# Performance work log

Measured on AMD Instinct MI355X. Metric: run time of the kernel, lower is better.

Reference implementation:

```python
import jax, jax.numpy as jnp
import numpy as np

B, T, D = 2, 2048, 2048
H, KVH, HD = 32, 8, 64
N_REP = H // KVH


def setup_inputs() -> dict:
    key = jax.random.key(0)
    ks = jax.random.split(key, 7)
    x = jax.random.normal(ks[0], (B, T, D), dtype=jnp.float32)
    # rope tables: [max_seq, head_dim//2]
    cos = jax.random.uniform(ks[1], (T, HD // 2), dtype=jnp.float32, minval=-1.0, maxval=1.0)
    sin = jax.random.uniform(ks[2], (T, HD // 2), dtype=jnp.float32, minval=-1.0, maxval=1.0)
    s = 0.02
    wq = jax.random.normal(ks[3], (D, H * HD), dtype=jnp.float32) * s
    wk = jax.random.normal(ks[4], (D, KVH * HD), dtype=jnp.float32) * s
    wv = jax.random.normal(ks[5], (D, KVH * HD), dtype=jnp.float32) * s
    wo = jax.random.normal(ks[6], (H * HD, D), dtype=jnp.float32) * s
    return {"x": x, "cos": cos, "sin": sin, "wq": wq, "wk": wk, "wv": wv, "wo": wo}


def _rotate(t):
    h = t.shape[-1] // 2
    return jnp.concatenate([-t[..., h:], t[..., :h]], axis=-1)


def reference(x, cos, sin, wq, wk, wv, wo):
    b, t, _ = x.shape
    # projections -> [B, heads, T, HD]
    q = (x @ wq).reshape(b, t, H, HD).transpose(0, 2, 1, 3)
    k = (x @ wk).reshape(b, t, KVH, HD).transpose(0, 2, 1, 3)
    v = (x @ wv).reshape(b, t, KVH, HD).transpose(0, 2, 1, 3)
    # rope: cos/sin tiled (concat) to full head_dim, broadcast over batch/head
    cos_f = jnp.tile(cos[:t], (1, 2))[None, None]  # [1,1,T,HD]
    sin_f = jnp.tile(sin[:t], (1, 2))[None, None]
    q = q * cos_f + _rotate(q) * sin_f
    k = k * cos_f + _rotate(k) * sin_f
    # GQA: repeat kv heads
    k = jnp.repeat(k, N_REP, axis=1)
    v = jnp.repeat(v, N_REP, axis=1)
    scale = 1.0 / np.sqrt(HD).astype(np.float32)
    scores = jnp.einsum('bhqd,bhkd->bhqk', q, k) * scale
    causal = jnp.tril(jnp.ones((t, t), dtype=bool))
    scores = jnp.where(causal, scores, jnp.float32(-1e30))
    attn = jax.nn.softmax(scores, axis=-1)
    out = jnp.einsum('bhqk,bhkd->bhqd', attn, v)
    out = out.transpose(0, 2, 1, 3).reshape(b, t, H * HD)
    return out @ wo
```

## Files before the change

kernel.cpp:

```cpp
#include <hip/hip_runtime.h>
#include <hip/hip_bf16.h>
#include <cstdint>

typedef unsigned short u16;
typedef unsigned int u32;
typedef __bf16 bf16x8 __attribute__((ext_vector_type(8)));
typedef float f32x4 __attribute__((ext_vector_type(4)));

#define BATCH 2
#define SEQ 2048
#define DMODEL 2048
#define NH 32
#define NKVH 8
#define HD 64
#define NQROWS (BATCH*SEQ)
#define QCOLS (NH*HD)
#define KVCOLS (NKVH*HD)
#define NCAT (QCOLS+2*KVCOLS)

static __device__ __forceinline__ u16 f2bf(float f) {
  u32 u = __float_as_uint(f);
  return (u16)((u + 0x7fffu + ((u >> 16) & 1u)) >> 16);
}

#define GLOAD16(gp, lp) __builtin_amdgcn_global_load_lds( \
    (const __attribute__((address_space(1))) void*)(gp),  \
    (__attribute__((address_space(3))) void*)(lp), 16, 0, 0)

__global__ __launch_bounds__(256) void k_cvt_bf16(const float* __restrict__ in,
                                                  u16* __restrict__ out, int n4) {
  int i = blockIdx.x * 256 + threadIdx.x;
  if (i >= n4) return;
  float4 v = reinterpret_cast<const float4*>(in)[i];
  ushort4 o;
  o.x = f2bf(v.x); o.y = f2bf(v.y); o.z = f2bf(v.z); o.w = f2bf(v.w);
  reinterpret_cast<ushort4*>(out)[i] = o;
}

__global__ __launch_bounds__(256) void k_transpose_w(const float* __restrict__ in,
                                                     u16* __restrict__ out, int R, int C) {
  __shared__ float tile[32][33];
  int c0 = blockIdx.x * 32, r0 = blockIdx.y * 32;
  int tx = threadIdx.x, ty = threadIdx.y;
#pragma unroll
  for (int i = 0; i < 4; i++)
    tile[ty * 4 + i][tx] = in[(size_t)(r0 + ty * 4 + i) * C + c0 + tx];
  __syncthreads();
#pragma unroll
  for (int i = 0; i < 4; i++)
    out[(size_t)(c0 + ty * 4 + i) * R + r0 + tx] = f2bf(tile[tx][ty * 4 + i]);
}

template<int EPI>
__global__ __launch_bounds__(256) void k_gemm(const u16* __restrict__ A,
                                              const u16* __restrict__ BT,
                                              void* __restrict__ Cout,
                                              int M, int N, int K,
                                              const float* __restrict__ cosb,
                                              const float* __restrict__ sinb,
                                              u16* __restrict__ dstK,
                                              u16* __restrict__ dstV) {
  __shared__ __align__(16) u16 As[128 * 32];
  __shared__ __align__(16) u16 Bs[128 * 32];
  const int tid = threadIdx.x;
  const int w = tid >> 6, l = tid & 63;
  const int l15 = l & 15, l4 = l >> 4;
  const int m0 = blockIdx.y * 128, n0 = blockIdx.x * 128;
  const int wr = w >> 1, wc = w & 1;

  const u16* ga = A + (size_t)(m0 + w * 32 + (l >> 2)) * K + (l & 3) * 8;
  const u16* gb = BT + (size_t)(n0 + w * 32 + (l >> 2)) * K + (l & 3) * 8;
  u16* asb = &As[w * 1024];
  u16* bsb = &Bs[w * 1024];
  const int af_off = (wr * 64 + l15) * 32 + l4 * 8;
  const int bf_off = (wc * 64 + l15) * 32 + l4 * 8;

  f32x4 acc[4][4] = {};
  for (int kt = 0; kt < K; kt += 32) {
    GLOAD16(ga, asb);
    GLOAD16(ga + 16 * (size_t)K, asb + 512);
    GLOAD16(gb, bsb);
    GLOAD16(gb + 16 * (size_t)K, bsb + 512);
    ga += 32; gb += 32;
    __syncthreads();
    bf16x8 af[4], bfv[4];
#pragma unroll
    for (int mi = 0; mi < 4; mi++)
      af[mi] = *reinterpret_cast<const bf16x8*>(&As[af_off + mi * 512]);
#pragma unroll
    for (int ni = 0; ni < 4; ni++)
      bfv[ni] = *reinterpret_cast<const bf16x8*>(&Bs[bf_off + ni * 512]);
#pragma unroll
    for (int mi = 0; mi < 4; mi++)
#pragma unroll
      for (int ni = 0; ni < 4; ni++)
        acc[mi][ni] = __builtin_amdgcn_mfma_f32_16x16x32_bf16(af[mi], bfv[ni], acc[mi][ni], 0, 0, 0);
    __syncthreads();
  }

  const int row0 = m0 + wr * 64 + l4 * 4;
  const int col0 = n0 + wc * 64 + l15;
  if constexpr (EPI == 1) {
    float* C = (float*)Cout;
#pragma unroll
    for (int mi = 0; mi < 4; mi++)
#pragma unroll
      for (int ni = 0; ni < 4; ni++)
#pragma unroll
        for (int j = 0; j < 4; j++)
          C[(size_t)(row0 + mi * 16 + j) * N + col0 + ni * 16] = acc[mi][ni][j];
  } else {
    if (n0 < QCOLS + KVCOLS) {
#pragma unroll
      for (int mi = 0; mi < 4; mi++)
#pragma unroll
        for (int j = 0; j < 4; j++) {
          int t = (row0 + mi * 16 + j) & (SEQ - 1);
#pragma unroll
          for (int ni = 0; ni < 2; ni++) {
            int d = ni * 16 + l15;
            float c = cosb[t * 32 + d], s = sinb[t * 32 + d];
            float a = acc[mi][ni][j], bb = acc[mi][ni + 2][j];
            acc[mi][ni][j]     = a * c - bb * s;
            acc[mi][ni + 2][j] = bb * c + a * s;
          }
        }
      if (n0 < QCOLS) {
        u16* C = (u16*)Cout;
#pragma unroll
        for (int mi = 0; mi < 4; mi++)
#pragma unroll
          for (int ni = 0; ni < 4; ni++)
#pragma unroll
            for (int j = 0; j < 4; j++)
              C[(size_t)(row0 + mi * 16 + j) * QCOLS + col0 + ni * 16] = f2bf(acc[mi][ni][j]);
      } else {
        int kc0 = col0 - QCOLS;
#pragma unroll
        for (int mi = 0; mi < 4; mi++)
#pragma unroll
          for (int ni = 0; ni < 4; ni++)
#pragma unroll
            for (int j = 0; j < 4; j++)
              dstK[(size_t)(row0 + mi * 16 + j) * KVCOLS + kc0 + ni * 16] = f2bf(acc[mi][ni][j]);
      }
    } else {
      int vc0 = col0 - (QCOLS + KVCOLS);
#pragma unroll
      for (int mi = 0; mi < 4; mi++) {
        int row = row0 + mi * 16;
        int b = row >> 11, t = row & (SEQ - 1);
#pragma unroll
        for (int ni = 0; ni < 4; ni++) {
          ushort4 v;
          v.x = f2bf(acc[mi][ni][0]);
          v.y = f2bf(acc[mi][ni][1]);
          v.z = f2bf(acc[mi][ni][2]);
          v.w = f2bf(acc[mi][ni][3]);
          *reinterpret_cast<ushort4*>(&dstV[((size_t)b * KVCOLS + vc0 + ni * 16) * SEQ + t]) = v;
        }
      }
    }
  }
}

__global__ __launch_bounds__(256) void k_attn(const u16* __restrict__ Q,
                                              const u16* __restrict__ K,
                                              const u16* __restrict__ VT,
                                              u16* __restrict__ AO) {
  __shared__ __align__(16) u16 Ks[2][4096];
  __shared__ __align__(16) u16 Vs[2][4096];
  __shared__ __align__(16) u16 Plds[4][16][72];
  const int tid = threadIdx.x;
  const int w = tid >> 6, l = tid & 63;
  const int l15 = l & 15, l4 = l >> 4;
  const int bh = blockIdx.y;
  const int b = bh >> 5, h = bh & 31, g = h >> 2;
  const float cS = 0.125f * 1.44269504088896f;
  const int srow_w = w * 8 + (l >> 3);
  const int sslot = l & 7;

  const u16* Kbase = K + ((size_t)b * SEQ) * KVCOLS + g * 64;
  const u16* Vbase = VT + ((size_t)(b * KVCOLS + g * 64)) * SEQ;

  for (int half = 0; half < 2; half++) {
    const int qt = half ? (31 - blockIdx.x) : blockIdx.x;
    const int qrow0 = qt * 64 + w * 16;
    const int nkc = qt + 1;

    bf16x8 aQ[2];
    {
      const u16* qp = Q + (size_t)(b * SEQ + qrow0 + l15) * QCOLS + h * 64 + l4 * 8;
      aQ[0] = *reinterpret_cast<const bf16x8*>(qp);
      aQ[1] = *reinterpret_cast<const bf16x8*>(qp + 32);
    }
    f32x4 oacc[4] = {};
    float lsumP[4] = {};

#pragma unroll
    for (int i = 0; i < 2; i++) {
      int r = i * 32 + srow_w;
      int cs = sslot ^ (r & 7);
      GLOAD16(Kbase + (size_t)r * KVCOLS + cs * 8, &Ks[0][i * 2048 + w * 512 + l * 8]);
      GLOAD16(Vbase + (size_t)r * SEQ + cs * 8, &Vs[0][i * 2048 + w * 512 + l * 8]);
    }
    __syncthreads();

    for (int kc = 0; kc < nkc; kc++) {
      const int bi = kc & 1;
      if (kc + 1 < nkc) {
#pragma unroll
        for (int i = 0; i < 2; i++) {
          int r = i * 32 + srow_w;
          int cs = sslot ^ (r & 7);
          GLOAD16(Kbase + (size_t)((kc + 1) * 64 + r) * KVCOLS + cs * 8,
                  &Ks[bi ^ 1][i * 2048 + w * 512 + l * 8]);
          GLOAD16(Vbase + (size_t)r * SEQ + (kc + 1) * 64 + cs * 8,
                  &Vs[bi ^ 1][i * 2048 + w * 512 + l * 8]);
        }
      }
      f32x4 sacc[4] = {};
#pragma unroll
      for (int ni = 0; ni < 4; ni++) {
        int kr = ni * 16 + l15;
#pragma unroll
        for (int hh = 0; hh < 2; hh++) {
          int slot = (hh * 4 + l4) ^ (kr & 7);
          bf16x8 kf = *reinterpret_cast<const bf16x8*>(&Ks[bi][kr * 64 + slot * 8]);
          sacc[ni] = __builtin_amdgcn_mfma_f32_16x16x32_bf16(aQ[hh], kf, sacc[ni], 0, 0, 0);
        }
      }
      const bool diag = (kc == qt);
      {
        int qr = qrow0 + l4 * 4;
#pragma unroll
        for (int ni = 0; ni < 4; ni++) {
          int kcol = kc * 64 + ni * 16 + l15;
#pragma unroll
          for (int j = 0; j < 4; j++) {
            float pv = exp2f(sacc[ni][j] * cS);
            if (diag && (kcol > qr + j)) pv = 0.f;
            lsumP[j] += pv;
            __bf16 pb = (__bf16)pv;
            Plds[w][l4 * 4 + j][ni * 16 + l15] = *(u16*)&pb;
          }
        }
      }
      {
        bf16x8 pa0 = *reinterpret_cast<const bf16x8*>(&Plds[w][l15][l4 * 8]);
        bf16x8 pa1 = *reinterpret_cast<const bf16x8*>(&Plds[w][l15][32 + l4 * 8]);
#pragma unroll
        for (int no = 0; no < 4; no++) {
          int vr = no * 16 + l15;
          int s0 = l4 ^ (vr & 7);
          int s1 = (4 + l4) ^ (vr & 7);
          bf16x8 v0 = *reinterpret_cast<const bf16x8*>(&Vs[bi][vr * 64 + s0 * 8]);
          bf16x8 v1 = *reinterpret_cast<const bf16x8*>(&Vs[bi][vr * 64 + s1 * 8]);
          oacc[no] = __builtin_amdgcn_mfma_f32_16x16x32_bf16(pa0, v0, oacc[no], 0, 0, 0);
          oacc[no] = __builtin_amdgcn_mfma_f32_16x16x32_bf16(pa1, v1, oacc[no], 0, 0, 0);
        }
      }
      __syncthreads();
    }
#pragma unroll
    for (int j = 0; j < 4; j++) {
      float v = lsumP[j];
      v += __shfl_xor(v, 1, 16);
      v += __shfl_xor(v, 2, 16);
      v += __shfl_xor(v, 4, 16);
      v += __shfl_xor(v, 8, 16);
      float rv = 1.f / v;
      int row = b * SEQ + qrow0 + l4 * 4 + j;
#pragma unroll
      for (int no = 0; no < 4; no++)
        AO[(size_t)row * QCOLS + h * 64 + no * 16 + l15] = f2bf(oacc[no][j] * rv);
    }
  }
}

extern "C" void kernel_launch(void* const* d_in, const int* in_sizes, int n_in,
                              void* d_out, int out_size, void* d_ws, size_t ws_size,
                              hipStream_t stream) {
  const float* x    = (const float*)d_in[0];
  const float* cosb = (const float*)d_in[1];
  const float* sinb = (const float*)d_in[2];
  const float* wq   = (const float*)d_in[3];
  const float* wk   = (const float*)d_in[4];
  const float* wv   = (const float*)d_in[5];
  const float* wo   = (const float*)d_in[6];
  float* out = (float*)d_out;

  char* ws = (char*)d_ws;
  size_t off = 0;
  auto alloc = [&](size_t bytes) -> void* {
    void* p = ws + off;
    off += (bytes + 255) & ~(size_t)255;
    return p;
  };
  u16* xb    = (u16*)alloc((size_t)NQROWS * DMODEL * 2);
  u16* wcatT = (u16*)alloc((size_t)NCAT * DMODEL * 2);
  u16* woT   = (u16*)alloc((size_t)DMODEL * QCOLS * 2);
  u16* Qb    = (u16*)alloc((size_t)NQROWS * QCOLS * 2);
  u16* Kb    = (u16*)alloc((size_t)NQROWS * KVCOLS * 2);
  u16* VTb   = (u16*)alloc((size_t)BATCH * KVCOLS * SEQ * 2);
  u16* AO    = (u16*)alloc((size_t)NQROWS * QCOLS * 2);

  k_cvt_bf16<<<dim3(NQROWS * DMODEL / 4 / 256), dim3(256), 0, stream>>>(x, xb, NQROWS * DMODEL / 4);
  k_transpose_w<<<dim3(QCOLS / 32, DMODEL / 32), dim3(32, 8), 0, stream>>>(wq, wcatT, DMODEL, QCOLS);
  k_transpose_w<<<dim3(KVCOLS / 32, DMODEL / 32), dim3(32, 8), 0, stream>>>(wk, wcatT + (size_t)QCOLS * DMODEL, DMODEL, KVCOLS);
  k_transpose_w<<<dim3(KVCOLS / 32, DMODEL / 32), dim3(32, 8), 0, stream>>>(wv, wcatT + (size_t)(QCOLS + KVCOLS) * DMODEL, DMODEL, KVCOLS);
  k_transpose_w<<<dim3(DMODEL / 32, QCOLS / 32), dim3(32, 8), 0, stream>>>(wo, woT, QCOLS, DMODEL);

  k_gemm<3><<<dim3(NCAT / 128, NQROWS / 128), 256, 0, stream>>>(
      xb, wcatT, Qb, NQROWS, NCAT, DMODEL, cosb, sinb, Kb, VTb);

  k_attn<<<dim3(16, BATCH * NH), 256, 0, stream>>>(Qb, Kb, VTb, AO);

  k_gemm<1><<<dim3(DMODEL / 128, NQROWS / 128), 256, 0, stream>>>(
      AO, woT, out, NQROWS, DMODEL, QCOLS, nullptr, nullptr, nullptr, nullptr);
}
```

Baseline: 245.8 us.

## Rewrite attention with 32x32 MFMA, register-resident P via permlane swap

The attention kernel moves from 16x16x32 to 32x32x16 bf16 MFMA, computing S transposed (K times Q) so each lane holds a column of probabilities. P is packed with v_cvt_pk_bf16_f32 and rearranged in registers with v_permlane32_swap, which removes the LDS round-trip for P. Q is pre-scaled once by the softmax constant, the block shrinks to 128 threads (2 waves of 32 query rows) with launch bounds for 3 blocks per CU, and MFMA sections get s_setprio hints. It relies on the MI355X-specific permlane32_swap instruction and adds rounding from scaling Q before the bf16 conversion. Like the previous kernel, it still uses exp2 without subtracting a running max.

```diff
diff --git a/kernel.cpp b/kernel.cpp
--- a/kernel.cpp
+++ b/kernel.cpp
@@ -6,6 +6,7 @@
 typedef unsigned int u32;
 typedef __bf16 bf16x8 __attribute__((ext_vector_type(8)));
 typedef float f32x4 __attribute__((ext_vector_type(4)));
+typedef float f32x16 __attribute__((ext_vector_type(16)));
 
 #define BATCH 2
 #define SEQ 2048
@@ -21,6 +22,9 @@
 static __device__ __forceinline__ u16 f2bf(float f) {
   u32 u = __float_as_uint(f);
   return (u16)((u + 0x7fffu + ((u >> 16) & 1u)) >> 16);
+}
+static __device__ __forceinline__ float bf2f(u16 h) {
+  return __uint_as_float(((u32)h) << 16);
 }
 
 #define GLOAD16(gp, lp) __builtin_amdgcn_global_load_lds( \
@@ -164,45 +168,51 @@
   }
 }
 
-__global__ __launch_bounds__(256) void k_attn(const u16* __restrict__ Q,
-                                              const u16* __restrict__ K,
-                                              const u16* __restrict__ VT,
-                                              u16* __restrict__ AO) {
+__global__ __launch_bounds__(128, 3) void k_attn(const u16* __restrict__ Q,
+                                                 const u16* __restrict__ K,
+                                                 const u16* __restrict__ VT,
+                                                 u16* __restrict__ AO) {
   __shared__ __align__(16) u16 Ks[2][4096];
   __shared__ __align__(16) u16 Vs[2][4096];
-  __shared__ __align__(16) u16 Plds[4][16][72];
   const int tid = threadIdx.x;
   const int w = tid >> 6, l = tid & 63;
-  const int l15 = l & 15, l4 = l >> 4;
+  const int lo = l & 31, hi = l >> 5;
   const int bh = blockIdx.y;
   const int b = bh >> 5, h = bh & 31, g = h >> 2;
-  const float cS = 0.125f * 1.44269504088896f;
-  const int srow_w = w * 8 + (l >> 3);
-  const int sslot = l & 7;
+  const float cS2 = 0.125f * 1.44269504088896f;
+  const int srow = l >> 3;
+  const int scol = l & 7;
 
   const u16* Kbase = K + ((size_t)b * SEQ) * KVCOLS + g * 64;
   const u16* Vbase = VT + ((size_t)(b * KVCOLS + g * 64)) * SEQ;
 
   for (int half = 0; half < 2; half++) {
     const int qt = half ? (31 - blockIdx.x) : blockIdx.x;
-    const int qrow0 = qt * 64 + w * 16;
+    const int qbase = qt * 64 + w * 32;
     const int nkc = qt + 1;
-
-    bf16x8 aQ[2];
+    const int qloc = w * 32 + lo;
+
+    bf16x8 qf[4];
     {
-      const u16* qp = Q + (size_t)(b * SEQ + qrow0 + l15) * QCOLS + h * 64 + l4 * 8;
-      aQ[0] = *reinterpret_cast<const bf16x8*>(qp);
-      aQ[1] = *reinterpret_cast<const bf16x8*>(qp + 32);
-    }
-    f32x4 oacc[4] = {};
-    float lsumP[4] = {};
-
-#pragma unroll
-    for (int i = 0; i < 2; i++) {
-      int r = i * 32 + srow_w;
-      int cs = sslot ^ (r & 7);
-      GLOAD16(Kbase + (size_t)r * KVCOLS + cs * 8, &Ks[0][i * 2048 + w * 512 + l * 8]);
-      GLOAD16(Vbase + (size_t)r * SEQ + cs * 8, &Vs[0][i * 2048 + w * 512 + l * 8]);
+      const u16* qp = Q + (size_t)(b * SEQ + qbase + lo) * QCOLS + h * 64 + hi * 8;
+#pragma unroll
+      for (int kb = 0; kb < 4; kb++) {
+        union { bf16x8 v; u16 s[8]; } in_, out_;
+        in_.v = *reinterpret_cast<const bf16x8*>(qp + kb * 16);
+#pragma unroll
+        for (int e = 0; e < 8; e++) out_.s[e] = f2bf(bf2f(in_.s[e]) * cS2);
+        qf[kb] = out_.v;
+      }
+    }
+    f32x16 oacc[2] = {};
+    float ls0 = 0.f, ls1 = 0.f;
+
+#pragma unroll
+    for (int i = 0; i < 4; i++) {
+      int r = w * 32 + i * 8 + srow;
+      int cs = scol ^ (srow & 7);
+      GLOAD16(Kbase + (size_t)r * KVCOLS + cs * 8, &Ks[0][(w * 32 + i * 8) * 64 + l * 8]);
+      GLOAD16(Vbase + (size_t)r * SEQ + cs * 8, &Vs[0][(w * 32 + i * 8) * 64 + l * 8]);
     }
     __syncthreads();
 
@@ -210,70 +220,87 @@
       const int bi = kc & 1;
       if (kc + 1 < nkc) {
 #pragma unroll
-        for (int i = 0; i < 2; i++) {
-          int r = i * 32 + srow_w;
-          int cs = sslot ^ (r & 7);
+        for (int i = 0; i < 4; i++) {
+          int r = w * 32 + i * 8 + srow;
+          int cs = scol ^ (srow & 7);
           GLOAD16(Kbase + (size_t)((kc + 1) * 64 + r) * KVCOLS + cs * 8,
-                  &Ks[bi ^ 1][i * 2048 + w * 512 + l * 8]);
+                  &Ks[bi ^ 1][(w * 32 + i * 8) * 64 + l * 8]);
           GLOAD16(Vbase + (size_t)r * SEQ + (kc + 1) * 64 + cs * 8,
-                  &Vs[bi ^ 1][i * 2048 + w * 512 + l * 8]);
-        }
-      }
-      f32x4 sacc[4] = {};
-#pragma unroll
-      for (int ni = 0; ni < 4; ni++) {
-        int kr = ni * 16 + l15;
-#pragma unroll
-        for (int hh = 0; hh < 2; hh++) {
-          int slot = (hh * 4 + l4) ^ (kr & 7);
-          bf16x8 kf = *reinterpret_cast<const bf16x8*>(&Ks[bi][kr * 64 + slot * 8]);
-          sacc[ni] = __builtin_amdgcn_mfma_f32_16x16x32_bf16(aQ[hh], kf, sacc[ni], 0, 0, 0);
-        }
-      }
+                  &Vs[bi ^ 1][(w * 32 + i * 8) * 64 + l * 8]);
+        }
+      }
+      f32x16 sacc[2] = {};
+      __builtin_amdgcn_s_setprio(1);
+#pragma unroll
+      for (int t = 0; t < 2; t++) {
+#pragma unroll
+        for (int kb = 0; kb < 4; kb++) {
+          int row = t * 32 + lo;
+          int slot = (2 * kb + hi) ^ (lo & 7);
+          bf16x8 kf = *reinterpret_cast<const bf16x8*>(&Ks[bi][row * 64 + slot * 8]);
+          sacc[t] = __builtin_amdgcn_mfma_f32_32x32x16_bf16(kf, qf[kb], sacc[t], 0, 0, 0);
+        }
+      }
+      __builtin_amdgcn_s_setprio(0);
+
       const bool diag = (kc == qt);
-      {
-        int qr = qrow0 + l4 * 4;
-#pragma unroll
-        for (int ni = 0; ni < 4; ni++) {
-          int kcol = kc * 64 + ni * 16 + l15;
-#pragma unroll
-          for (int j = 0; j < 4; j++) {
-            float pv = exp2f(sacc[ni][j] * cS);
-            if (diag && (kcol > qr + j)) pv = 0.f;
-            lsumP[j] += pv;
-            __bf16 pb = (__bf16)pv;
-            Plds[w][l4 * 4 + j][ni * 16 + l15] = *(u16*)&pb;
+      u32 u[2][4][2];
+#pragma unroll
+      for (int t = 0; t < 2; t++) {
+        float pv[16];
+#pragma unroll
+        for (int r = 0; r < 16; r++) {
+          float e = exp2f(sacc[t][r]);
+          if (diag) {
+            int kvoff = t * 32 + (r & 3) + 8 * (r >> 2) + 4 * hi;
+            if (kvoff > qloc) e = 0.f;
           }
-        }
-      }
-      {
-        bf16x8 pa0 = *reinterpret_cast<const bf16x8*>(&Plds[w][l15][l4 * 8]);
-        bf16x8 pa1 = *reinterpret_cast<const bf16x8*>(&Plds[w][l15][32 + l4 * 8]);
-#pragma unroll
-        for (int no = 0; no < 4; no++) {
-          int vr = no * 16 + l15;
-          int s0 = l4 ^ (vr & 7);
-          int s1 = (4 + l4) ^ (vr & 7);
-          bf16x8 v0 = *reinterpret_cast<const bf16x8*>(&Vs[bi][vr * 64 + s0 * 8]);
-          bf16x8 v1 = *reinterpret_cast<const bf16x8*>(&Vs[bi][vr * 64 + s1 * 8]);
-          oacc[no] = __builtin_amdgcn_mfma_f32_16x16x32_bf16(pa0, v0, oacc[no], 0, 0, 0);
-          oacc[no] = __builtin_amdgcn_mfma_f32_16x16x32_bf16(pa1, v1, oacc[no], 0, 0, 0);
-        }
+          pv[r] = e;
+          if (t == 0) ls0 += e; else ls1 += e;
+        }
+#pragma unroll
+        for (int qd = 0; qd < 4; qd++)
+#pragma unroll
+          for (int hh = 0; hh < 2; hh++) {
+            u32 uu;
+            asm("v_cvt_pk_bf16_f32 %0, %1, %2"
+                : "=v"(uu) : "v"(pv[qd * 4 + 2 * hh]), "v"(pv[qd * 4 + 2 * hh + 1]));
+            u[t][qd][hh] = uu;
+          }
+      }
+
+#pragma unroll
+      for (int km = 0; km < 4; km++) {
+        const int t = km >> 1, p = km & 1;
+        u32 a0 = u[t][2 * p][0], b0 = u[t][2 * p + 1][0];
+        u32 a1 = u[t][2 * p][1], b1 = u[t][2 * p + 1][1];
+        asm("v_permlane32_swap_b32 %0, %1" : "+v"(a0), "+v"(b0));
+        asm("v_permlane32_swap_b32 %0, %1" : "+v"(a1), "+v"(b1));
+        union { u32 uu[4]; bf16x8 v; } pa;
+        pa.uu[0] = a0; pa.uu[1] = a1; pa.uu[2] = b0; pa.uu[3] = b1;
+        __builtin_amdgcn_s_setprio(1);
+#pragma unroll
+        for (int td = 0; td < 2; td++) {
+          int row = td * 32 + lo;
+          int slot = (2 * km + hi) ^ (lo & 7);
+          bf16x8 vf = *reinterpret_cast<const bf16x8*>(&Vs[bi][row * 64 + slot * 8]);
+          oacc[td] = __builtin_amdgcn_mfma_f32_32x32x16_bf16(pa.v, vf, oacc[td], 0, 0, 0);
+        }
+        __builtin_amdgcn_s_setprio(0);
       }
       __syncthreads();
     }
-#pragma unroll
-    for (int j = 0; j < 4; j++) {
-      float v = lsumP[j];
-      v += __shfl_xor(v, 1, 16);
-      v += __shfl_xor(v, 2, 16);
-      v += __shfl_xor(v, 4, 16);
-      v += __shfl_xor(v, 8, 16);
-      float rv = 1.f / v;
-      int row = b * SEQ + qrow0 + l4 * 4 + j;
-#pragma unroll
-      for (int no = 0; no < 4; no++)
-        AO[(size_t)row * QCOLS + h * 64 + no * 16 + l15] = f2bf(oacc[no][j] * rv);
+
+    float tot = ls0 + ls1;
+    tot += __shfl_xor(tot, 32);
+#pragma unroll
+    for (int r = 0; r < 16; r++) {
+      int qr = (r & 3) + 8 * (r >> 2) + 4 * hi;
+      float den = __shfl(tot, qr);
+      float rv = __builtin_amdgcn_rcpf(den);
+      size_t rowbase = (size_t)(b * SEQ + qt * 64 + w * 32 + qr) * QCOLS + h * 64 + lo;
+      AO[rowbase]      = f2bf(oacc[0][r] * rv);
+      AO[rowbase + 32] = f2bf(oacc[1][r] * rv);
     }
   }
 }
@@ -314,7 +341,7 @@
   k_gemm<3><<<dim3(NCAT / 128, NQROWS / 128), 256, 0, stream>>>(
       xb, wcatT, Qb, NQROWS, NCAT, DMODEL, cosb, sinb, Kb, VTb);
 
-  k_attn<<<dim3(16, BATCH * NH), 256, 0, stream>>>(Qb, Kb, VTb, AO);
+  k_attn<<<dim3(16, BATCH * NH), 128, 0, stream>>>(Qb, Kb, VTb, AO);
 
   k_gemm<1><<<dim3(DMODEL / 128, NQROWS / 128), 256, 0, stream>>>(
       AO, woT, out, NQROWS, DMODEL, QCOLS, nullptr, nullptr, nullptr, nullptr);
```

New measurement: 231.5 us. 1.06x faster.
